# Optimization experiments

Measured on AMD Instinct MI355X. Metric: run time of the kernel, lower is better.

Reference implementation:

```python
import jax, jax.numpy as jnp
import numpy as np

DIM, H, K, RADIUS = 128, 4, 32, 0.3
DH = DIM // H
N, M = 16384, 4096


def setup_inputs() -> dict:
    key = jax.random.key(0)
    ks = jax.random.split(key, 16)
    s = 0.02
    return {
        "xyz": jax.random.normal(ks[0], (N, 3), jnp.float32),
        "feats": jax.random.normal(ks[1], (N, DIM), jnp.float32),
        "idx_center": jax.random.randint(ks[2], (M,), 0, N, jnp.int64),
        "Wq": jax.random.normal(ks[3], (DIM, DIM), jnp.float32) * s,
        "Wk": jax.random.normal(ks[4], (DIM, DIM), jnp.float32) * s,
        "Wv": jax.random.normal(ks[5], (DIM, DIM), jnp.float32) * s,
        "Wo": jax.random.normal(ks[6], (DIM, DIM), jnp.float32) * s,
        "bo": jnp.zeros((DIM,), jnp.float32),
        "g1": jnp.ones((DIM,), jnp.float32),
        "be1": jnp.zeros((DIM,), jnp.float32),
        "g2": jnp.ones((DIM,), jnp.float32),
        "be2": jnp.zeros((DIM,), jnp.float32),
        "W1": jax.random.normal(ks[7], (4 * DIM, DIM), jnp.float32) * s,
        "b1f": jnp.zeros((4 * DIM,), jnp.float32),
        "W2": jax.random.normal(ks[8], (DIM, 4 * DIM), jnp.float32) * s,
        "b2f": jnp.zeros((DIM,), jnp.float32),
    }


def _layernorm(x, g, b, eps=1e-5):
    mu = x.mean(-1, keepdims=True)
    var = ((x - mu) ** 2).mean(-1, keepdims=True)
    return (x - mu) / jnp.sqrt(var + eps) * g + b


def reference(xyz, feats, idx_center, Wq, Wk, Wv, Wo, bo, g1, be1, g2, be2, W1, b1f, W2, b2f):
    m = idx_center.shape[0]
    c_xyz = xyz[idx_center]          # (M,3)
    c_feat = feats[idx_center]       # (M,DIM)
    # pairwise Euclidean distance (M,N), like torch.cdist
    d2 = (jnp.sum(c_xyz * c_xyz, -1)[:, None] + jnp.sum(xyz * xyz, -1)[None, :]
          - 2.0 * (c_xyz @ xyz.T))
    dist = jnp.sqrt(jnp.maximum(d2, 1e-12))
    mask = dist < RADIUS
    mask = mask.at[jnp.arange(m), idx_center].set(True)  # force self-inclusion
    dmask = jnp.where(mask, dist, jnp.inf)
    neg_d, nbr_idx = jax.lax.top_k(-dmask, K)            # k smallest distances
    nbr_dist = -neg_d
    valid = jnp.isfinite(nbr_dist)                       # (M,K)
    nbr_feats = jnp.where(valid[..., None], feats[nbr_idx], 0.0)  # (M,K,DIM)
    # tiny per-center attention
    q = (c_feat @ Wq.T).reshape(m, H, DH)
    k = (nbr_feats @ Wk.T).reshape(m, K, H, DH).transpose(0, 2, 1, 3)  # (M,H,K,DH)
    v = (nbr_feats @ Wv.T).reshape(m, K, H, DH).transpose(0, 2, 1, 3)
    attn = jnp.einsum('mhd,mhkd->mhk', q * (DH ** -0.5), k)
    attn = jnp.where(valid[:, None, :], attn, -1e9)
    attn = jax.nn.softmax(attn, axis=-1)
    out = jnp.einsum('mhk,mhkd->mhd', attn, v)
    out = out.transpose(0, 2, 1).reshape(m, DIM)  # matches torch transpose(1,2).reshape
    upd = out @ Wo.T + bo
    c_feat = c_feat + _layernorm(upd, g1, be1)
    ffn = jax.nn.relu(c_feat @ W1.T + b1f) @ W2.T + b2f
    c_feat = c_feat + _layernorm(ffn, g2, be2)
    nearest = jnp.argmin(dist, axis=0)            # (N,) nearest center per point
    return feats + c_feat[nearest]
```

## Files before the change

kernel.cpp:

```cpp
#include <hip/hip_runtime.h>
#include <hip/hip_bf16.h>

#define DIMF 128
#define KNBR 32
#define NH 4
#define DH 32
#define RADIUS 0.3f
#define CB 8
#define CAND 256
#define PPB 32

#define PACK_BLOCKS 60

typedef unsigned long long u64t;

__device__ __forceinline__ void tr4_tile(const float4* __restrict__ in4, float4* __restrict__ out4,
                                         int AI, int BI, int a0, int b0, int t, char* smem) {
    float4(*tile)[33] = (float4(*)[33])smem;
    int tx = t & 31, ty = t >> 5;
    for (int r = ty; r < 32; r += 8) tile[r][tx] = in4[(long)(b0 + r) * AI + a0 + tx];
    __syncthreads();
    for (int r = ty; r < 32; r += 8) out4[(long)(a0 + r) * BI + b0 + tx] = tile[tx][r];
}

__global__ __launch_bounds__(256) void pack_kernel(
    const float* __restrict__ Wq, const float* __restrict__ Wv,
    const float* __restrict__ Wo, const float* __restrict__ W1,
    const float* __restrict__ W2, const float* __restrict__ Wk,
    float4* __restrict__ qp4, float4* __restrict__ vp4, float4* __restrict__ op4,
    float4* __restrict__ w1p4, float4* __restrict__ w2p4, float4* __restrict__ kp4) {
    __shared__ __align__(16) char smem[16896];
    int pk = blockIdx.x, t = threadIdx.x;
    if (pk < 4) {
        tr4_tile((const float4*)Wq, qp4, 32, 128, 0, pk * 32, t, smem);
    } else if (pk < 8) {
        tr4_tile((const float4*)Wv, vp4, 32, 128, 0, (pk - 4) * 32, t, smem);
    } else if (pk < 12) {
        tr4_tile((const float4*)Wo, op4, 32, 128, 0, (pk - 8) * 32, t, smem);
    } else if (pk < 28) {
        tr4_tile((const float4*)W1, w1p4, 32, 512, 0, (pk - 12) * 32, t, smem);
    } else if (pk < 44) {
        int i = pk - 28;
        tr4_tile((const float4*)W2, w2p4, 128, 128, (i >> 2) * 32, (i & 3) * 32, t, smem);
    } else {
        int idx = (pk - 44) * 256 + t;
        int q = idx >> 7, j = idx & 127;
        float4 w;
        w.x = Wk[(long)(4 * q + 0) * DIMF + j];
        w.y = Wk[(long)(4 * q + 1) * DIMF + j];
        w.z = Wk[(long)(4 * q + 2) * DIMF + j];
        w.w = Wk[(long)(4 * q + 3) * DIMF + j];
        kp4[q * DIMF + j] = w;
    }
}

__global__ __launch_bounds__(256) void main_kernel(
    const float* __restrict__ xyz, const float* __restrict__ feats,
    const int* __restrict__ idxc,
    const float4* __restrict__ qp4, const float4* __restrict__ kp4,
    const float4* __restrict__ vp4, const float4* __restrict__ op4,
    const float* __restrict__ bo, const float* __restrict__ g1,
    const float* __restrict__ be1, const float* __restrict__ g2,
    const float* __restrict__ be2, const float4* __restrict__ w1p4,
    const float* __restrict__ b1f, const float4* __restrict__ w2p4,
    const float* __restrict__ b2f, float* __restrict__ cfin,
    int* __restrict__ bestm, int N, int M) {
    __shared__ __align__(16) char smem[32768];
    __shared__ int nbrl[CB][KNBR];
    __shared__ int cnt[CB];

    int t = threadIdx.x;
    int b = blockIdx.x;
    int nAttn = M / CB;

    if (b >= nAttn) {
        float4* cds = (float4*)smem;
        int pt = t >> 3, q = t & 7;
        int n = (b - nAttn) * PPB + pt;
        float px = xyz[3 * n], py = xyz[3 * n + 1], pz = xyz[3 * n + 2];
        float bd0 = INFINITY, bd1 = INFINITY;
        int bm0 = 0, bm1 = 0;
        for (int c0 = 0; c0 < M; c0 += 1024) {
            __syncthreads();
            for (int i = t; i < 1024; i += 256) {
                int ic = idxc[c0 + i];
                float cx = xyz[3 * ic], cy = xyz[3 * ic + 1], cz = xyz[3 * ic + 2];
                cds[i] = make_float4(-2.0f * cx, -2.0f * cy, -2.0f * cz,
                                     (cx * cx + cy * cy) + cz * cz);
            }
            __syncthreads();
#pragma unroll 8
            for (int i = 0; i < 64; ++i) {
                int ci0 = q + (2 * i) * 8, ci1 = q + (2 * i + 1) * 8;
                float4 ca = cds[ci0];
                float4 cb = cds[ci1];
                float sa = fmaf(ca.x, px, fmaf(ca.y, py, fmaf(ca.z, pz, ca.w)));
                float sb = fmaf(cb.x, px, fmaf(cb.y, py, fmaf(cb.z, pz, cb.w)));
                if (sa < bd0) { bd0 = sa; bm0 = c0 + ci0; }
                if (sb < bd1) { bd1 = sb; bm1 = c0 + ci1; }
            }
        }
        if (bd1 < bd0 || (bd1 == bd0 && bm1 < bm0)) { bd0 = bd1; bm0 = bm1; }
#pragma unroll
        for (int o = 1; o < 8; o <<= 1) {
            float obd = __shfl_xor(bd0, o);
            int obm = __shfl_xor(bm0, o);
            if (obd < bd0 || (obd == bd0 && obm < bm0)) { bd0 = obd; bm0 = obm; }
        }
        if (q == 0) bestm[n] = bm0;
        return;
    }

    int m0 = b * CB;

    {
        u64t(*cand)[CAND] = (u64t(*)[CAND])smem;
        if (t < CB) cnt[t] = 0;
        __syncthreads();
        float nx[CB], ny[CB], nz[CB], cw[CB];
#pragma unroll
        for (int tc = 0; tc < CB; ++tc) {
            int ic = idxc[m0 + tc];
            float cx = xyz[3 * ic], cy = xyz[3 * ic + 1], cz = xyz[3 * ic + 2];
            cw[tc] = (cx * cx + cy * cy) + cz * cz;
            nx[tc] = -2.0f * cx; ny[tc] = -2.0f * cy; nz[tc] = -2.0f * cz;
        }
        const float R2 = RADIUS * RADIUS;
        for (int n = t; n < N; n += 256) {
            float x = xyz[3 * n], y = xyz[3 * n + 1], z = xyz[3 * n + 2];
            float pw = (x * x + y * y) + z * z;
            float rhs = R2 - pw;
#pragma unroll
            for (int tc = 0; tc < CB; ++tc) {
                float s = fmaf(nx[tc], x, fmaf(ny[tc], y, fmaf(nz[tc], z, cw[tc])));
                if (s < rhs) {
                    int pos = atomicAdd(&cnt[tc], 1);
                    if (pos < CAND)
                        cand[tc][pos] = (((u64t)__float_as_uint(fmaxf(s + pw, 0.0f))) << 32) | (unsigned)n;
                }
            }
        }
        __syncthreads();
        int w = t >> 6, lane = t & 63;
        for (int rep = 0; rep < 2; ++rep) {
            int cidx = w + rep * 4;
            int C = cnt[cidx] < CAND ? cnt[cidx] : CAND;
            const u64t* vc = cand[cidx];
            if (C <= 64) {
                u64t mykey = (lane < C) ? vc[lane] : ~0ull;
                int rank = 0;
                for (int j = 0; j < C; ++j) rank += (vc[j] < mykey) ? 1 : 0;
                if (lane < C && rank < KNBR) nbrl[cidx][rank] = (int)(mykey & 0xffffffffu);
                if (lane >= C && lane < KNBR) nbrl[cidx][lane] = -1;
            } else {
                u64t mykey[4];
                int myrank[4];
#pragma unroll
                for (int s = 0; s < 4; ++s) {
                    int i = s * 64 + lane;
                    mykey[s] = (i < C) ? vc[i] : ~0ull;
                    myrank[s] = 0;
                }
                for (int j = 0; j < C; ++j) {
                    u64t kj = vc[j];
#pragma unroll
                    for (int s = 0; s < 4; ++s) myrank[s] += (kj < mykey[s]) ? 1 : 0;
                }
#pragma unroll
                for (int s = 0; s < 4; ++s) {
                    int i = s * 64 + lane;
                    if (i < C && myrank[s] < KNBR) nbrl[cidx][myrank[s]] = (int)(mykey[s] & 0xffffffffu);
                }
            }
        }
    }
    __syncthreads();

    float(*cf)[DIMF] = (float(*)[DIMF])smem;
    float(*cf2)[DIMF] = (float(*)[DIMF])(smem + 4096);
    float(*S1)[4 * DIMF] = (float(*)[4 * DIMF])(smem + 8192);
    float(*S2)[DIMF] = (float(*)[DIMF])(smem + 24576);
    float(*S3)[DIMF] = (float(*)[DIMF])(smem + 28672);

    int lane127 = t & 127;
    int cg = (t >> 7) * 4;
    int c8 = t >> 5, k32 = t & 31;

    {
        int ic = idxc[m0 + c8];
        *(float4*)&cf[c8][k32 * 4] = *(const float4*)&feats[(long)ic * DIMF + k32 * 4];
    }
    __syncthreads();

    {
        float acc[4] = {0.f, 0.f, 0.f, 0.f};
        for (int jj = 0; jj < 32; ++jj) {
            float4 w = qp4[jj * DIMF + lane127];
#pragma unroll
            for (int cc = 0; cc < 4; ++cc) {
                float4 x = *(const float4*)&cf[cg + cc][jj * 4];
                acc[cc] += w.x * x.x + w.y * x.y + w.z * x.z + w.w * x.w;
            }
        }
#pragma unroll
        for (int cc = 0; cc < 4; ++cc) S2[cg + cc][lane127] = acc[cc] * 0.17677669529663687f;
    }
    __syncthreads();

    {
        int j = lane127, hs = t >> 7;
#pragma unroll
        for (int hh = 0; hh < 2; ++hh) {
            int h = hs * 2 + hh;
            float acc[8] = {0.f, 0.f, 0.f, 0.f, 0.f, 0.f, 0.f, 0.f};
            for (int d4 = 0; d4 < 8; ++d4) {
                float4 w = kp4[(h * 8 + d4) * DIMF + j];
#pragma unroll
                for (int c = 0; c < 8; ++c) {
                    float4 qv = *(const float4*)&S2[c][h * DH + d4 * 4];
                    acc[c] += qv.x * w.x + qv.y * w.y + qv.z * w.z + qv.w * w.w;
                }
            }
#pragma unroll
            for (int c = 0; c < 8; ++c) S1[c][h * DIMF + j] = acc[c];
        }
    }
    __syncthreads();

    {
        int ni = nbrl[c8][k32];
        const float* nrow = feats + (long)(ni < 0 ? 0 : ni) * DIMF;
        float lg[4] = {0.f, 0.f, 0.f, 0.f};
        for (int jj = 0; jj < 32; ++jj) {
            float4 f = *(const float4*)&nrow[jj * 4];
#pragma unroll
            for (int h = 0; h < 4; ++h) {
                float4 qwv = *(const float4*)&S1[c8][h * DIMF + jj * 4];
                lg[h] += f.x * qwv.x + f.y * qwv.y + f.z * qwv.z + f.w * qwv.w;
            }
        }
        if (ni < 0) { lg[0] = -1e9f; lg[1] = -1e9f; lg[2] = -1e9f; lg[3] = -1e9f; }
#pragma unroll
        for (int h = 0; h < 4; ++h) {
            float mx = lg[h];
            for (int o = 16; o; o >>= 1) mx = fmaxf(mx, __shfl_xor(mx, o, 32));
            float e = expf(lg[h] - mx);
            float s = e;
            for (int o = 16; o; o >>= 1) s += __shfl_xor(s, o, 32);
            S3[c8][h * KNBR + k32] = e / s;
        }
    }
    __syncthreads();

    {
        int j4 = k32 * 4;
        float a0x = 0.f, a0y = 0.f, a0z = 0.f, a0w = 0.f;
        float a1x = 0.f, a1y = 0.f, a1z = 0.f, a1w = 0.f;
        float a2x = 0.f, a2y = 0.f, a2z = 0.f, a2w = 0.f;
        float a3x = 0.f, a3y = 0.f, a3z = 0.f, a3w = 0.f;
        for (int k = 0; k < KNBR; ++k) {
            int ni = nbrl[c8][k];
            const float* nrow = feats + (long)(ni < 0 ? 0 : ni) * DIMF;
            float4 f = *(const float4*)&nrow[j4];
            float w0 = S3[c8][0 * KNBR + k], w1 = S3[c8][1 * KNBR + k];
            float w2 = S3[c8][2 * KNBR + k], w3 = S3[c8][3 * KNBR + k];
            a0x += w0 * f.x; a0y += w0 * f.y; a0z += w0 * f.z; a0w += w0 * f.w;
            a1x += w1 * f.x; a1y += w1 * f.y; a1z += w1 * f.z; a1w += w1 * f.w;
            a2x += w2 * f.x; a2y += w2 * f.y; a2z += w2 * f.z; a2w += w2 * f.w;
            a3x += w3 * f.x; a3y += w3 * f.y; a3z += w3 * f.z; a3w += w3 * f.w;
        }
        __syncthreads();
        *(float4*)&S1[c8][0 * DIMF + j4] = make_float4(a0x, a0y, a0z, a0w);
        *(float4*)&S1[c8][1 * DIMF + j4] = make_float4(a1x, a1y, a1z, a1w);
        *(float4*)&S1[c8][2 * DIMF + j4] = make_float4(a2x, a2y, a2z, a2w);
        *(float4*)&S1[c8][3 * DIMF + j4] = make_float4(a3x, a3y, a3z, a3w);
    }
    __syncthreads();

    {
        int i = lane127, h = i >> 5, d = i & 31;
        float acc[4] = {0.f, 0.f, 0.f, 0.f};
        for (int jj = 0; jj < 32; ++jj) {
            float4 w = vp4[jj * DIMF + i];
#pragma unroll
            for (int cc = 0; cc < 4; ++cc) {
                float4 pv = *(const float4*)&S1[cg + cc][h * DIMF + jj * 4];
                acc[cc] += w.x * pv.x + w.y * pv.y + w.z * pv.z + w.w * pv.w;
            }
        }
        __syncthreads();
#pragma unroll
        for (int cc = 0; cc < 4; ++cc) S2[cg + cc][d * NH + h] = acc[cc];
    }
    __syncthreads();

    {
        int i = lane127;
        float acc[4] = {0.f, 0.f, 0.f, 0.f};
        for (int jj = 0; jj < 32; ++jj) {
            float4 w = op4[jj * DIMF + i];
#pragma unroll
            for (int cc = 0; cc < 4; ++cc) {
                float4 x = *(const float4*)&S2[cg + cc][jj * 4];
                acc[cc] += w.x * x.x + w.y * x.y + w.z * x.z + w.w * x.w;
            }
        }
        float b = bo[i];
        __syncthreads();
#pragma unroll
        for (int cc = 0; cc < 4; ++cc) S3[cg + cc][i] = acc[cc] + b;
    }
    __syncthreads();

    {
        int i4 = k32 * 4;
        float4 u = *(const float4*)&S3[c8][i4];
        float s = ((u.x + u.y) + u.z) + u.w;
        for (int o = 16; o; o >>= 1) s += __shfl_xor(s, o, 32);
        float mu = s * (1.0f / DIMF);
        float d0 = u.x - mu, d1 = u.y - mu, d2 = u.z - mu, d3 = u.w - mu;
        float vs = ((d0 * d0 + d1 * d1) + d2 * d2) + d3 * d3;
        for (int o = 16; o; o >>= 1) vs += __shfl_xor(vs, o, 32);
        float rs = 1.0f / sqrtf(vs * (1.0f / DIMF) + 1e-5f);
        float4 g = *(const float4*)&g1[i4];
        float4 b = *(const float4*)&be1[i4];
        float4 base = *(const float4*)&cf[c8][i4];
        float4 r;
        r.x = base.x + d0 * rs * g.x + b.x;
        r.y = base.y + d1 * rs * g.y + b.y;
        r.z = base.z + d2 * rs * g.z + b.z;
        r.w = base.w + d3 * rs * g.w + b.w;
        *(float4*)&cf2[c8][i4] = r;
    }
    __syncthreads();

    {
        int u0 = lane127;
        float acc[4][4];
#pragma unroll
        for (int p = 0; p < 4; ++p)
#pragma unroll
            for (int cc = 0; cc < 4; ++cc) acc[p][cc] = 0.f;
        for (int jj = 0; jj < 32; ++jj) {
            float4 x[4];
#pragma unroll
            for (int cc = 0; cc < 4; ++cc) x[cc] = *(const float4*)&cf2[cg + cc][jj * 4];
#pragma unroll
            for (int p = 0; p < 4; ++p) {
                float4 w = w1p4[jj * 512 + u0 + p * DIMF];
#pragma unroll
                for (int cc = 0; cc < 4; ++cc)
                    acc[p][cc] += w.x * x[cc].x + w.y * x[cc].y + w.z * x[cc].z + w.w * x[cc].w;
            }
        }
#pragma unroll
        for (int p = 0; p < 4; ++p) {
            float b = b1f[u0 + p * DIMF];
#pragma unroll
            for (int cc = 0; cc < 4; ++cc)
                S1[cg + cc][u0 + p * DIMF] = fmaxf(acc[p][cc] + b, 0.f);
        }
    }
    __syncthreads();

    {
        int i = lane127;
        float acc[4] = {0.f, 0.f, 0.f, 0.f};
        for (int uu = 0; uu < 128; ++uu) {
            float4 w = w2p4[uu * DIMF + i];
#pragma unroll
            for (int cc = 0; cc < 4; ++cc) {
                float4 hh = *(const float4*)&S1[cg + cc][uu * 4];
                acc[cc] += w.x * hh.x + w.y * hh.y + w.z * hh.z + w.w * hh.w;
            }
        }
        float b = b2f[i];
        __syncthreads();
#pragma unroll
        for (int cc = 0; cc < 4; ++cc) S3[cg + cc][i] = acc[cc] + b;
    }
    __syncthreads();

    {
        int i4 = k32 * 4;
        float4 u = *(const float4*)&S3[c8][i4];
        float s = ((u.x + u.y) + u.z) + u.w;
        for (int o = 16; o; o >>= 1) s += __shfl_xor(s, o, 32);
        float mu = s * (1.0f / DIMF);
        float d0 = u.x - mu, d1 = u.y - mu, d2 = u.z - mu, d3 = u.w - mu;
        float vs = ((d0 * d0 + d1 * d1) + d2 * d2) + d3 * d3;
        for (int o = 16; o; o >>= 1) vs += __shfl_xor(vs, o, 32);
        float rs = 1.0f / sqrtf(vs * (1.0f / DIMF) + 1e-5f);
        float4 g = *(const float4*)&g2[i4];
        float4 b = *(const float4*)&be2[i4];
        float4 base = *(const float4*)&cf2[c8][i4];
        float4 r;
        r.x = base.x + d0 * rs * g.x + b.x;
        r.y = base.y + d1 * rs * g.y + b.y;
        r.z = base.z + d2 * rs * g.z + b.z;
        r.w = base.w + d3 * rs * g.w + b.w;
        *(float4*)&cfin[(long)(m0 + c8) * DIMF + i4] = r;
    }
}

__global__ __launch_bounds__(256) void out_kernel(const float4* __restrict__ feats4,
                                                  const float* __restrict__ cfin,
                                                  const int* __restrict__ bestm,
                                                  float4* __restrict__ out4, int total) {
    int idx = blockIdx.x * 256 + threadIdx.x;
    if (idx >= total) return;
    int n = idx >> 5, c = idx & 31;
    const float4* cf4 = (const float4*)cfin;
    float4 f = feats4[idx];
    float4 g = cf4[(long)bestm[n] * 32 + c];
    out4[idx] = make_float4(f.x + g.x, f.y + g.y, f.z + g.z, f.w + g.w);
}

extern "C" void kernel_launch(void* const* d_in, const int* in_sizes, int n_in,
                              void* d_out, int out_size, void* d_ws, size_t ws_size,
                              hipStream_t stream) {
    const float* xyz = (const float*)d_in[0];
    const float* feats = (const float*)d_in[1];
    const int* idxc = (const int*)d_in[2];
    const float* Wq = (const float*)d_in[3];
    const float* Wk = (const float*)d_in[4];
    const float* Wv = (const float*)d_in[5];
    const float* Wo = (const float*)d_in[6];
    const float* bo = (const float*)d_in[7];
    const float* g1 = (const float*)d_in[8];
    const float* be1 = (const float*)d_in[9];
    const float* g2 = (const float*)d_in[10];
    const float* be2 = (const float*)d_in[11];
    const float* W1 = (const float*)d_in[12];
    const float* b1f = (const float*)d_in[13];
    const float* W2 = (const float*)d_in[14];
    const float* b2f = (const float*)d_in[15];

    int N = in_sizes[0] / 3;
    int M = in_sizes[2];

    char* ws = (char*)d_ws;
    size_t off = 0;
    float* cfin = (float*)(ws + off); off += (size_t)M * DIMF * 4;
    int* bestm = (int*)(ws + off); off += (size_t)N * 4;
    float4* qp4 = (float4*)(ws + off); off += (size_t)DIMF * DIMF * 4;
    float4* vp4 = (float4*)(ws + off); off += (size_t)DIMF * DIMF * 4;
    float4* op4 = (float4*)(ws + off); off += (size_t)DIMF * DIMF * 4;
    float4* kp4 = (float4*)(ws + off); off += (size_t)DIMF * DIMF * 4;
    float4* w1p4 = (float4*)(ws + off); off += (size_t)4 * DIMF * DIMF * 4;
    float4* w2p4 = (float4*)(ws + off); off += (size_t)4 * DIMF * DIMF * 4;
    (void)ws_size; (void)n_in; (void)out_size;

    pack_kernel<<<PACK_BLOCKS, 256, 0, stream>>>(
        Wq, Wv, Wo, W1, W2, Wk, qp4, vp4, op4, w1p4, w2p4, kp4);
    main_kernel<<<M / CB + N / PPB, 256, 0, stream>>>(
        xyz, feats, idxc, qp4, kp4, vp4, op4, bo, g1, be1, g2, be2,
        w1p4, b1f, w2p4, b2f, cfin, bestm, N, M);
    out_kernel<<<(N * DIMF / 4 + 255) / 256, 256, 0, stream>>>(
        (const float4*)feats, cfin, bestm, (float4*)d_out, N * DIMF / 4);
}
```

Measured before the change: 189.8 us.

## Double main kernel block size to 512 threads and repartition per-stage work

Raises the main kernel's block size from 256 to 512 threads. Each attention/FFN stage now gives each thread fewer centers or heads, and the nearest-center blocks process 64 points each. This is meant to shorten the per-block serial chain through the radius scan, ranking and small matmuls by exposing more parallel threads. The cost is less per-thread weight reuse and more barrier participants, and __launch_bounds__(512,8) caps registers per thread, which may cause spills.

```diff
diff --git a/kernel.cpp b/kernel.cpp
--- a/kernel.cpp
+++ b/kernel.cpp
@@ -8,7 +8,8 @@
 #define RADIUS 0.3f
 #define CB 8
 #define CAND 256
-#define PPB 32
+#define PPB 64
+#define TMAIN 512
 
 #define PACK_BLOCKS 60
 
@@ -54,7 +55,7 @@
     }
 }
 
-__global__ __launch_bounds__(256) void main_kernel(
+__global__ __launch_bounds__(512, 8) void main_kernel(
     const float* __restrict__ xyz, const float* __restrict__ feats,
     const int* __restrict__ idxc,
     const float4* __restrict__ qp4, const float4* __restrict__ kp4,
@@ -82,7 +83,7 @@
         int bm0 = 0, bm1 = 0;
         for (int c0 = 0; c0 < M; c0 += 1024) {
             __syncthreads();
-            for (int i = t; i < 1024; i += 256) {
+            for (int i = t; i < 1024; i += TMAIN) {
                 int ic = idxc[c0 + i];
                 float cx = xyz[3 * ic], cy = xyz[3 * ic + 1], cz = xyz[3 * ic + 2];
                 cds[i] = make_float4(-2.0f * cx, -2.0f * cy, -2.0f * cz,
@@ -126,7 +127,7 @@
             nx[tc] = -2.0f * cx; ny[tc] = -2.0f * cy; nz[tc] = -2.0f * cz;
         }
         const float R2 = RADIUS * RADIUS;
-        for (int n = t; n < N; n += 256) {
+        for (int n = t; n < N; n += TMAIN) {
             float x = xyz[3 * n], y = xyz[3 * n + 1], z = xyz[3 * n + 2];
             float pw = (x * x + y * y) + z * z;
             float rhs = R2 - pw;
@@ -142,8 +143,8 @@
         }
         __syncthreads();
         int w = t >> 6, lane = t & 63;
-        for (int rep = 0; rep < 2; ++rep) {
-            int cidx = w + rep * 4;
+        {
+            int cidx = w;
             int C = cnt[cidx] < CAND ? cnt[cidx] : CAND;
             const u64t* vc = cand[cidx];
             if (C <= 64) {
@@ -182,137 +183,133 @@
     float(*S2)[DIMF] = (float(*)[DIMF])(smem + 24576);
     float(*S3)[DIMF] = (float(*)[DIMF])(smem + 28672);
 
-    int lane127 = t & 127;
-    int cg = (t >> 7) * 4;
-    int c8 = t >> 5, k32 = t & 31;
-
-    {
-        int ic = idxc[m0 + c8];
-        *(float4*)&cf[c8][k32 * 4] = *(const float4*)&feats[(long)ic * DIMF + k32 * 4];
-    }
-    __syncthreads();
-
-    {
-        float acc[4] = {0.f, 0.f, 0.f, 0.f};
+    if (t < 256) {
+        int c8t = t >> 5, k32t = t & 31;
+        int ic = idxc[m0 + c8t];
+        *(float4*)&cf[c8t][k32t * 4] = *(const float4*)&feats[(long)ic * DIMF + k32t * 4];
+    }
+    __syncthreads();
+
+    {
+        int i = t & 127, cpair = (t >> 7) * 2;
+        float acc0 = 0.f, acc1 = 0.f;
         for (int jj = 0; jj < 32; ++jj) {
-            float4 w = qp4[jj * DIMF + lane127];
-#pragma unroll
-            for (int cc = 0; cc < 4; ++cc) {
-                float4 x = *(const float4*)&cf[cg + cc][jj * 4];
-                acc[cc] += w.x * x.x + w.y * x.y + w.z * x.z + w.w * x.w;
-            }
-        }
-#pragma unroll
-        for (int cc = 0; cc < 4; ++cc) S2[cg + cc][lane127] = acc[cc] * 0.17677669529663687f;
-    }
-    __syncthreads();
-
-    {
-        int j = lane127, hs = t >> 7;
-#pragma unroll
-        for (int hh = 0; hh < 2; ++hh) {
-            int h = hs * 2 + hh;
-            float acc[8] = {0.f, 0.f, 0.f, 0.f, 0.f, 0.f, 0.f, 0.f};
-            for (int d4 = 0; d4 < 8; ++d4) {
-                float4 w = kp4[(h * 8 + d4) * DIMF + j];
-#pragma unroll
-                for (int c = 0; c < 8; ++c) {
-                    float4 qv = *(const float4*)&S2[c][h * DH + d4 * 4];
-                    acc[c] += qv.x * w.x + qv.y * w.y + qv.z * w.z + qv.w * w.w;
-                }
-            }
-#pragma unroll
-            for (int c = 0; c < 8; ++c) S1[c][h * DIMF + j] = acc[c];
-        }
-    }
-    __syncthreads();
-
-    {
+            float4 w = qp4[jj * DIMF + i];
+            float4 x0 = *(const float4*)&cf[cpair][jj * 4];
+            float4 x1 = *(const float4*)&cf[cpair + 1][jj * 4];
+            acc0 += w.x * x0.x + w.y * x0.y + w.z * x0.z + w.w * x0.w;
+            acc1 += w.x * x1.x + w.y * x1.y + w.z * x1.z + w.w * x1.w;
+        }
+        S2[cpair][i] = acc0 * 0.17677669529663687f;
+        S2[cpair + 1][i] = acc1 * 0.17677669529663687f;
+    }
+    __syncthreads();
+
+    {
+        int j = t & 127, h = t >> 7;
+        float acc[8] = {0.f, 0.f, 0.f, 0.f, 0.f, 0.f, 0.f, 0.f};
+        for (int d4 = 0; d4 < 8; ++d4) {
+            float4 w = kp4[(h * 8 + d4) * DIMF + j];
+#pragma unroll
+            for (int c = 0; c < 8; ++c) {
+                float4 qv = *(const float4*)&S2[c][h * DH + d4 * 4];
+                acc[c] += qv.x * w.x + qv.y * w.y + qv.z * w.z + qv.w * w.w;
+            }
+        }
+#pragma unroll
+        for (int c = 0; c < 8; ++c) S1[c][h * DIMF + j] = acc[c];
+    }
+    __syncthreads();
+
+    {
+        int c8 = t >> 6, hh = (t >> 5) & 1, k32 = t & 31;
+        int h0 = hh * 2, h1 = hh * 2 + 1;
         int ni = nbrl[c8][k32];
         const float* nrow = feats + (long)(ni < 0 ? 0 : ni) * DIMF;
-        float lg[4] = {0.f, 0.f, 0.f, 0.f};
+        float lg0 = 0.f, lg1 = 0.f;
         for (int jj = 0; jj < 32; ++jj) {
             float4 f = *(const float4*)&nrow[jj * 4];
-#pragma unroll
-            for (int h = 0; h < 4; ++h) {
-                float4 qwv = *(const float4*)&S1[c8][h * DIMF + jj * 4];
-                lg[h] += f.x * qwv.x + f.y * qwv.y + f.z * qwv.z + f.w * qwv.w;
-            }
-        }
-        if (ni < 0) { lg[0] = -1e9f; lg[1] = -1e9f; lg[2] = -1e9f; lg[3] = -1e9f; }
-#pragma unroll
-        for (int h = 0; h < 4; ++h) {
-            float mx = lg[h];
+            float4 qa = *(const float4*)&S1[c8][h0 * DIMF + jj * 4];
+            float4 qb = *(const float4*)&S1[c8][h1 * DIMF + jj * 4];
+            lg0 += f.x * qa.x + f.y * qa.y + f.z * qa.z + f.w * qa.w;
+            lg1 += f.x * qb.x + f.y * qb.y + f.z * qb.z + f.w * qb.w;
+        }
+        if (ni < 0) { lg0 = -1e9f; lg1 = -1e9f; }
+        {
+            float mx = lg0;
             for (int o = 16; o; o >>= 1) mx = fmaxf(mx, __shfl_xor(mx, o, 32));
-            float e = expf(lg[h] - mx);
+            float e = expf(lg0 - mx);
             float s = e;
             for (int o = 16; o; o >>= 1) s += __shfl_xor(s, o, 32);
-            S3[c8][h * KNBR + k32] = e / s;
-        }
-    }
-    __syncthreads();
-
-    {
-        int j4 = k32 * 4;
+            S3[c8][h0 * KNBR + k32] = e / s;
+        }
+        {
+            float mx = lg1;
+            for (int o = 16; o; o >>= 1) mx = fmaxf(mx, __shfl_xor(mx, o, 32));
+            float e = expf(lg1 - mx);
+            float s = e;
+            for (int o = 16; o; o >>= 1) s += __shfl_xor(s, o, 32);
+            S3[c8][h1 * KNBR + k32] = e / s;
+        }
+    }
+    __syncthreads();
+
+    {
+        int c8 = t >> 6, hh = (t >> 5) & 1, j32 = t & 31;
+        int j4 = j32 * 4;
+        int h0 = hh * 2, h1 = hh * 2 + 1;
         float a0x = 0.f, a0y = 0.f, a0z = 0.f, a0w = 0.f;
         float a1x = 0.f, a1y = 0.f, a1z = 0.f, a1w = 0.f;
-        float a2x = 0.f, a2y = 0.f, a2z = 0.f, a2w = 0.f;
-        float a3x = 0.f, a3y = 0.f, a3z = 0.f, a3w = 0.f;
         for (int k = 0; k < KNBR; ++k) {
             int ni = nbrl[c8][k];
             const float* nrow = feats + (long)(ni < 0 ? 0 : ni) * DIMF;
             float4 f = *(const float4*)&nrow[j4];
-            float w0 = S3[c8][0 * KNBR + k], w1 = S3[c8][1 * KNBR + k];
-            float w2 = S3[c8][2 * KNBR + k], w3 = S3[c8][3 * KNBR + k];
+            float w0 = S3[c8][h0 * KNBR + k], w1 = S3[c8][h1 * KNBR + k];
             a0x += w0 * f.x; a0y += w0 * f.y; a0z += w0 * f.z; a0w += w0 * f.w;
             a1x += w1 * f.x; a1y += w1 * f.y; a1z += w1 * f.z; a1w += w1 * f.w;
-            a2x += w2 * f.x; a2y += w2 * f.y; a2z += w2 * f.z; a2w += w2 * f.w;
-            a3x += w3 * f.x; a3y += w3 * f.y; a3z += w3 * f.z; a3w += w3 * f.w;
-        }
-        __syncthreads();
-        *(float4*)&S1[c8][0 * DIMF + j4] = make_float4(a0x, a0y, a0z, a0w);
-        *(float4*)&S1[c8][1 * DIMF + j4] = make_float4(a1x, a1y, a1z, a1w);
-        *(float4*)&S1[c8][2 * DIMF + j4] = make_float4(a2x, a2y, a2z, a2w);
-        *(float4*)&S1[c8][3 * DIMF + j4] = make_float4(a3x, a3y, a3z, a3w);
-    }
-    __syncthreads();
-
-    {
-        int i = lane127, h = i >> 5, d = i & 31;
-        float acc[4] = {0.f, 0.f, 0.f, 0.f};
+        }
+        __syncthreads();
+        *(float4*)&S1[c8][h0 * DIMF + j4] = make_float4(a0x, a0y, a0z, a0w);
+        *(float4*)&S1[c8][h1 * DIMF + j4] = make_float4(a1x, a1y, a1z, a1w);
+    }
+    __syncthreads();
+
+    {
+        int i = t & 127, cpair = (t >> 7) * 2;
+        int h = i >> 5, d = i & 31;
+        float acc0 = 0.f, acc1 = 0.f;
         for (int jj = 0; jj < 32; ++jj) {
             float4 w = vp4[jj * DIMF + i];
-#pragma unroll
-            for (int cc = 0; cc < 4; ++cc) {
-                float4 pv = *(const float4*)&S1[cg + cc][h * DIMF + jj * 4];
-                acc[cc] += w.x * pv.x + w.y * pv.y + w.z * pv.z + w.w * pv.w;
-            }
-        }
-        __syncthreads();
-#pragma unroll
-        for (int cc = 0; cc < 4; ++cc) S2[cg + cc][d * NH + h] = acc[cc];
-    }
-    __syncthreads();
-
-    {
-        int i = lane127;
-        float acc[4] = {0.f, 0.f, 0.f, 0.f};
+            float4 p0 = *(const float4*)&S1[cpair][h * DIMF + jj * 4];
+            float4 p1 = *(const float4*)&S1[cpair + 1][h * DIMF + jj * 4];
+            acc0 += w.x * p0.x + w.y * p0.y + w.z * p0.z + w.w * p0.w;
+            acc1 += w.x * p1.x + w.y * p1.y + w.z * p1.z + w.w * p1.w;
+        }
+        __syncthreads();
+        S2[cpair][d * NH + h] = acc0;
+        S2[cpair + 1][d * NH + h] = acc1;
+    }
+    __syncthreads();
+
+    {
+        int i = t & 127, cpair = (t >> 7) * 2;
+        float acc0 = 0.f, acc1 = 0.f;
         for (int jj = 0; jj < 32; ++jj) {
             float4 w = op4[jj * DIMF + i];
-#pragma unroll
-            for (int cc = 0; cc < 4; ++cc) {
-                float4 x = *(const float4*)&S2[cg + cc][jj * 4];
-                acc[cc] += w.x * x.x + w.y * x.y + w.z * x.z + w.w * x.w;
-            }
-        }
-        float b = bo[i];
-        __syncthreads();
-#pragma unroll
-        for (int cc = 0; cc < 4; ++cc) S3[cg + cc][i] = acc[cc] + b;
-    }
-    __syncthreads();
-
-    {
+            float4 x0 = *(const float4*)&S2[cpair][jj * 4];
+            float4 x1 = *(const float4*)&S2[cpair + 1][jj * 4];
+            acc0 += w.x * x0.x + w.y * x0.y + w.z * x0.z + w.w * x0.w;
+            acc1 += w.x * x1.x + w.y * x1.y + w.z * x1.z + w.w * x1.w;
+        }
+        float bb = bo[i];
+        __syncthreads();
+        S3[cpair][i] = acc0 + bb;
+        S3[cpair + 1][i] = acc1 + bb;
+    }
+    __syncthreads();
+
+    if (t < 256) {
+        int c8 = t >> 5, k32 = t & 31;
         int i4 = k32 * 4;
         float4 u = *(const float4*)&S3[c8][i4];
         float s = ((u.x + u.y) + u.z) + u.w;
@@ -335,53 +332,42 @@
     __syncthreads();
 
     {
-        int u0 = lane127;
-        float acc[4][4];
-#pragma unroll
-        for (int p = 0; p < 4; ++p)
-#pragma unroll
-            for (int cc = 0; cc < 4; ++cc) acc[p][cc] = 0.f;
+        int u0 = t & 127, p = t >> 7;
+        int u = p * DIMF + u0;
+        float acc[8] = {0.f, 0.f, 0.f, 0.f, 0.f, 0.f, 0.f, 0.f};
         for (int jj = 0; jj < 32; ++jj) {
-            float4 x[4];
-#pragma unroll
-            for (int cc = 0; cc < 4; ++cc) x[cc] = *(const float4*)&cf2[cg + cc][jj * 4];
-#pragma unroll
-            for (int p = 0; p < 4; ++p) {
-                float4 w = w1p4[jj * 512 + u0 + p * DIMF];
-#pragma unroll
-                for (int cc = 0; cc < 4; ++cc)
-                    acc[p][cc] += w.x * x[cc].x + w.y * x[cc].y + w.z * x[cc].z + w.w * x[cc].w;
-            }
-        }
-#pragma unroll
-        for (int p = 0; p < 4; ++p) {
-            float b = b1f[u0 + p * DIMF];
-#pragma unroll
-            for (int cc = 0; cc < 4; ++cc)
-                S1[cg + cc][u0 + p * DIMF] = fmaxf(acc[p][cc] + b, 0.f);
-        }
-    }
-    __syncthreads();
-
-    {
-        int i = lane127;
-        float acc[4] = {0.f, 0.f, 0.f, 0.f};
+            float4 w = w1p4[jj * 512 + u];
+#pragma unroll
+            for (int c = 0; c < 8; ++c) {
+                float4 x = *(const float4*)&cf2[c][jj * 4];
+                acc[c] += w.x * x.x + w.y * x.y + w.z * x.z + w.w * x.w;
+            }
+        }
+        float bb = b1f[u];
+#pragma unroll
+        for (int c = 0; c < 8; ++c) S1[c][u] = fmaxf(acc[c] + bb, 0.f);
+    }
+    __syncthreads();
+
+    {
+        int i = t & 127, cpair = (t >> 7) * 2;
+        float acc0 = 0.f, acc1 = 0.f;
         for (int uu = 0; uu < 128; ++uu) {
             float4 w = w2p4[uu * DIMF + i];
-#pragma unroll
-            for (int cc = 0; cc < 4; ++cc) {
-                float4 hh = *(const float4*)&S1[cg + cc][uu * 4];
-                acc[cc] += w.x * hh.x + w.y * hh.y + w.z * hh.z + w.w * hh.w;
-            }
-        }
-        float b = b2f[i];
-        __syncthreads();
-#pragma unroll
-        for (int cc = 0; cc < 4; ++cc) S3[cg + cc][i] = acc[cc] + b;
-    }
-    __syncthreads();
-
-    {
+            float4 h0v = *(const float4*)&S1[cpair][uu * 4];
+            float4 h1v = *(const float4*)&S1[cpair + 1][uu * 4];
+            acc0 += w.x * h0v.x + w.y * h0v.y + w.z * h0v.z + w.w * h0v.w;
+            acc1 += w.x * h1v.x + w.y * h1v.y + w.z * h1v.z + w.w * h1v.w;
+        }
+        float bb = b2f[i];
+        __syncthreads();
+        S3[cpair][i] = acc0 + bb;
+        S3[cpair + 1][i] = acc1 + bb;
+    }
+    __syncthreads();
+
+    if (t < 256) {
+        int c8 = t >> 5, k32 = t & 31;
         int i4 = k32 * 4;
         float4 u = *(const float4*)&S3[c8][i4];
         float s = ((u.x + u.y) + u.z) + u.w;
@@ -453,7 +439,7 @@
 
     pack_kernel<<<PACK_BLOCKS, 256, 0, stream>>>(
         Wq, Wv, Wo, W1, W2, Wk, qp4, vp4, op4, w1p4, w2p4, kp4);
-    main_kernel<<<M / CB + N / PPB, 256, 0, stream>>>(
+    main_kernel<<<M / CB + N / PPB, TMAIN, 0, stream>>>(
         xyz, feats, idxc, qp4, kp4, vp4, op4, bo, g1, be1, g2, be2,
         w1p4, b1f, w2p4, b2f, cfin, bestm, N, M);
     out_kernel<<<(N * DIMF / 4 + 255) / 256, 256, 0, stream>>>(
```

Measured after the change: 229.5 us. 20.9% more time.
